# Optimization experiments

Measured on AMD Instinct MI355X. Metric: run time of the kernel, lower is better.

## Reference

```python
import jax, jax.numpy as jnp
import numpy as np

B, T, D, H = 4, 2048, 2048, 16
HD = D // H

def setup_inputs() -> dict:
    key = jax.random.key(0)
    k1, k2, k3 = jax.random.split(key, 3)
    x = jax.random.normal(k1, (B, T, D), dtype=jnp.float32)
    mask = jnp.ones((B, T), dtype=jnp.int32)
    # torch Linear weights, scaled like default init (~1/sqrt(fan_in))
    w_qkv = jax.random.normal(k2, (3 * D, D), dtype=jnp.float32) / np.sqrt(D)
    w_o = jax.random.normal(k3, (D, D), dtype=jnp.float32) / np.sqrt(D)
    return {"x": x, "mask": mask, "w_qkv": w_qkv, "w_o": w_o}

def reference(x, mask, w_qkv, w_o):
    # qkv projection: (B,T,D) @ (D,3D) -> (B,T,3D)
    qkv = jnp.einsum('btd,ed->bte', x, w_qkv)
    q, k, v = jnp.split(qkv, 3, axis=-1)
    # (B,T,D) -> (B,H,T,HD)
    def to_heads(t):
        return t.reshape(B, T, H, HD).transpose(0, 2, 1, 3)
    q, k, v = to_heads(q), to_heads(k), to_heads(v)
    scale = 1.0 / np.sqrt(HD).astype(np.float32)
    att = jnp.einsum('bhqd,bhkd->bhqk', q, k) * scale  # (B,H,T,T)
    att = jnp.where(mask[:, None, None, :] == 0, -jnp.inf, att)
    att = jax.nn.softmax(att, axis=-1)
    y = jnp.einsum('bhqk,bhkd->bhqd', att, v)  # (B,H,T,HD)
    y = y.transpose(0, 2, 1, 3).reshape(B, T, D)
    return jnp.einsum('btd,ed->bte', y, w_o)
```

## Files before the change

### kernel.cpp

```cpp
#include <hip/hip_runtime.h>
#include <hip/hip_bf16.h>

typedef __bf16 bf16;
typedef bf16 bf16x8 __attribute__((ext_vector_type(8)));
typedef float f32x4 __attribute__((ext_vector_type(4)));

struct alignas(8) bh4 { bf16 v[4]; };

__device__ __forceinline__ void glds16(const bf16* g, bf16* l) {
  __builtin_amdgcn_global_load_lds(
      (const __attribute__((address_space(1))) void*)g,
      (__attribute__((address_space(3))) void*)l, 16, 0, 0);
}

#define QSCALE (1.4426950408889634f / 11.313708498984761f)
#define DEFER_THR 8.0f

__global__ void convert_to_bf16(const float* __restrict__ s, bf16* __restrict__ dst,
                                long n) {
  const long stride = (long)gridDim.x * blockDim.x * 8;
  for (long i = ((long)blockIdx.x * blockDim.x + threadIdx.x) * 8; i < n; i += stride) {
    float4 a = *(const float4*)(s + i);
    float4 b = *(const float4*)(s + i + 4);
    bf16x8 o;
    o[0] = (bf16)a.x; o[1] = (bf16)a.y; o[2] = (bf16)a.z; o[3] = (bf16)a.w;
    o[4] = (bf16)b.x; o[5] = (bf16)b.y; o[6] = (bf16)b.z; o[7] = (bf16)b.w;
    *(bf16x8*)(dst + i) = o;
  }
}

template <int MODE>
__global__ void gemm_bt(const bf16* __restrict__ A, const bf16* __restrict__ Bw,
                        void* __restrict__ C0v, bf16* __restrict__ C1,
                        bf16* __restrict__ C2, int M, int N, int K) {
  __shared__ __align__(16) bf16 sA[128 * 32];
  __shared__ __align__(16) bf16 sB[128 * 32];
  const int tid = threadIdx.x;
  const int lane = tid & 63, wid = tid >> 6;
  const int wm = wid & 1, wn = wid >> 1;
  const int quad = lane >> 4, l16 = lane & 15;
  const int bm = blockIdx.y * 128, bn = blockIdx.x * 128;

  f32x4 acc[4][4] = {};

  const int srow = tid >> 2, scol = (tid & 3) << 3;
  const bf16* gA = A + (size_t)(bm + srow) * K + scol;
  const bf16* gB = Bw + (size_t)(bn + srow) * K + scol;
  const size_t row64 = (size_t)64 * K;

  for (int k0 = 0; k0 < K; k0 += 32) {
    glds16(gA + k0, &sA[tid * 8]);
    glds16(gA + k0 + row64, &sA[2048 + tid * 8]);
    glds16(gB + k0, &sB[tid * 8]);
    glds16(gB + k0 + row64, &sB[2048 + tid * 8]);
    __syncthreads();
    bf16x8 af[4], bff[4];
#pragma unroll
    for (int mt = 0; mt < 4; ++mt)
      af[mt] = *(const bf16x8*)&sA[(wm * 64 + mt * 16 + l16) * 32 + quad * 8];
#pragma unroll
    for (int nt = 0; nt < 4; ++nt)
      bff[nt] = *(const bf16x8*)&sB[(wn * 64 + nt * 16 + l16) * 32 + quad * 8];
#pragma unroll
    for (int mt = 0; mt < 4; ++mt)
#pragma unroll
      for (int nt = 0; nt < 4; ++nt)
        acc[mt][nt] = __builtin_amdgcn_mfma_f32_16x16x32_bf16(af[mt], bff[nt], acc[mt][nt], 0, 0, 0);
    __syncthreads();
  }

  if (MODE == 0) {
    bf16* C0 = (bf16*)C0v;
    const int which = blockIdx.x >> 4;
    const int h = blockIdx.x & 15;
#pragma unroll
    for (int mt = 0; mt < 4; ++mt) {
      const int m0 = bm + wm * 64 + mt * 16 + quad * 4;
      const int b = m0 >> 11, t0 = m0 & 2047;
#pragma unroll
      for (int nt = 0; nt < 4; ++nt) {
        const int hd = wn * 64 + nt * 16 + l16;
        if (which == 0) {
          bf16* dst = C0 + (((size_t)(b * 16 + h) * 2048 + t0) * 128 + hd);
#pragma unroll
          for (int r = 0; r < 4; ++r) dst[(size_t)r * 128] = (bf16)(acc[mt][nt][r] * QSCALE);
        } else if (which == 1) {
          bf16* dst = C1 + (((size_t)(b * 16 + h) * 2048 + t0) * 128 + hd);
#pragma unroll
          for (int r = 0; r < 4; ++r) dst[(size_t)r * 128] = (bf16)acc[mt][nt][r];
        } else {
          bh4 pk;
#pragma unroll
          for (int r = 0; r < 4; ++r) pk.v[r] = (bf16)acc[mt][nt][r];
          *(bh4*)(C2 + ((size_t)((b * 16 + h) * 128 + hd) * 2048 + t0)) = pk;
        }
      }
    }
  } else {
    float* C0 = (float*)C0v;
#pragma unroll
    for (int mt = 0; mt < 4; ++mt) {
      const int m0 = bm + wm * 64 + mt * 16 + quad * 4;
#pragma unroll
      for (int nt = 0; nt < 4; ++nt) {
        const int n = bn + wn * 64 + nt * 16 + l16;
#pragma unroll
        for (int r = 0; r < 4; ++r)
          C0[(size_t)(m0 + r) * N + n] = acc[mt][nt][r];
      }
    }
  }
}

__global__ __launch_bounds__(256, 3)
void attn_kernel(const bf16* __restrict__ Q, const bf16* __restrict__ Kb,
                 const bf16* __restrict__ Vt, const int* __restrict__ mask,
                 bf16* __restrict__ Y) {
  __shared__ __align__(16) bf16 smem[25600];
  bf16* sK = smem;
  bf16* sV = smem + 8192;
  bf16* sP = smem + 16384;

  const int tid = threadIdx.x;
  const int lane = tid & 63, w = tid >> 6;
  const int quad = lane >> 4, l16 = lane & 15;
  const int bh = blockIdx.x, b = bh >> 4, h = bh & 15;
  const int qt = blockIdx.y;
  const size_t head = (size_t)bh * (2048 * 128);

  bf16x8 qf[2][4];
#pragma unroll
  for (int nt = 0; nt < 2; ++nt) {
    const int t = qt * 128 + w * 32 + nt * 16 + l16;
    const bf16* g = Q + head + (size_t)t * 128 + quad * 8;
#pragma unroll
    for (int kk = 0; kk < 4; ++kk)
      qf[nt][kk] = *(const bf16x8*)(g + kk * 32);
  }

  f32x4 o[8][2] = {};
  float mrow[2] = {-3.0e38f, -3.0e38f};
  float lrow[2] = {0.0f, 0.0f};

  const int* maskb = mask + b * 2048;
  bf16* sPw = sP + w * (32 * 72);

  unsigned long long vmask;
  {
    const int4* mp4 = (const int4*)maskb;
    bool ok = true;
#pragma unroll
    for (int j = 0; j < 8; ++j) {
      const int4 q4 = mp4[lane * 8 + j];
      ok = ok && (q4.x != 0) && (q4.y != 0) && (q4.z != 0) && (q4.w != 0);
    }
    vmask = __ballot(ok);
  }

  for (int kt = 0; kt < 32; ++kt) {
    const int key0 = kt * 64;
    {
      const int cp = lane & 15;
      const int rbase = w * 16 + (lane >> 4);
#pragma unroll
      for (int p = 0; p < 4; ++p) {
        const int row = rbase + p * 4;
        const int c = (cp & 8) | ((cp ^ row) & 7);
        glds16(Kb + head + (size_t)(key0 + row) * 128 + c * 8,
               &sK[(w * 16 + p * 4) * 128 + lane * 8]);
      }
    }
    {
      const int cp = lane & 7;
      const int rbase = w * 32 + (lane >> 3);
#pragma unroll
      for (int p = 0; p < 4; ++p) {
        const int row = rbase + p * 8;
        const int c = cp ^ (row & 7);
        glds16(Vt + head + (size_t)row * 2048 + key0 + c * 8,
               &sV[(w * 32 + p * 8) * 64 + lane * 8]);
      }
    }
    __syncthreads();

    f32x4 st[4][2] = {};
#pragma unroll
    for (int kk = 0; kk < 4; ++kk) {
      bf16x8 ak[4];
#pragma unroll
      for (int mt = 0; mt < 4; ++mt) {
        const int row = mt * 16 + l16;
        const int c = kk * 4 + quad;
        const int cp = (c & 8) | ((c ^ row) & 7);
        ak[mt] = *(const bf16x8*)&sK[row * 128 + cp * 8];
      }
#pragma unroll
      for (int mt = 0; mt < 4; ++mt)
#pragma unroll
        for (int nt = 0; nt < 2; ++nt)
          st[mt][nt] = __builtin_amdgcn_mfma_f32_16x16x32_bf16(ak[mt], qf[nt][kk], st[mt][nt], 0, 0, 0);
    }

    if (((vmask >> (2 * kt)) & 3ULL) != 3ULL) {
#pragma unroll
      for (int mt = 0; mt < 4; ++mt) {
#pragma unroll
        for (int r = 0; r < 4; ++r) {
          const int mk = maskb[key0 + mt * 16 + quad * 4 + r];
#pragma unroll
          for (int nt = 0; nt < 2; ++nt)
            if (mk == 0) { st[mt][nt][r] = -1.0e30f; }
        }
      }
    }

#pragma unroll
    for (int nt = 0; nt < 2; ++nt) {
      float mx = -1.0e30f;
#pragma unroll
      for (int mt = 0; mt < 4; ++mt)
#pragma unroll
        for (int r = 0; r < 4; ++r) mx = fmaxf(mx, st[mt][nt][r]);
      mx = fmaxf(mx, __shfl_xor(mx, 16));
      mx = fmaxf(mx, __shfl_xor(mx, 32));
      if (!__all(mx <= mrow[nt] + DEFER_THR)) {
        const float newm = fmaxf(mrow[nt], mx);
        const float alpha = exp2f(mrow[nt] - newm);
        mrow[nt] = newm;
        lrow[nt] *= alpha;
#pragma unroll
        for (int mt = 0; mt < 8; ++mt)
#pragma unroll
          for (int r = 0; r < 4; ++r) o[mt][nt][r] *= alpha;
      }
      const float m = mrow[nt];
      float rs = 0.0f;
#pragma unroll
      for (int mt = 0; mt < 4; ++mt) {
        bh4 pk;
#pragma unroll
        for (int r = 0; r < 4; ++r) {
          const float p = exp2f(st[mt][nt][r] - m);
          rs += p;
          pk.v[r] = (bf16)p;
        }
        *(bh4*)&sPw[(nt * 16 + l16) * 72 + mt * 16 + quad * 4] = pk;
      }
      rs += __shfl_xor(rs, 16);
      rs += __shfl_xor(rs, 32);
      lrow[nt] += rs;
    }

#pragma unroll
    for (int kk = 0; kk < 2; ++kk) {
      bf16x8 bp[2];
#pragma unroll
      for (int nt = 0; nt < 2; ++nt)
        bp[nt] = *(const bf16x8*)&sPw[(nt * 16 + l16) * 72 + kk * 32 + quad * 8];
#pragma unroll
      for (int mt = 0; mt < 8; ++mt) {
        const int row = mt * 16 + l16;
        const int c = kk * 4 + quad;
        bf16x8 av = *(const bf16x8*)&sV[row * 64 + (c ^ (row & 7)) * 8];
#pragma unroll
        for (int nt = 0; nt < 2; ++nt)
          o[mt][nt] = __builtin_amdgcn_mfma_f32_16x16x32_bf16(av, bp[nt], o[mt][nt], 0, 0, 0);
      }
    }
    __syncthreads();
  }

  bf16* sOw = smem + w * 4352;
#pragma unroll
  for (int nt = 0; nt < 2; ++nt) {
    const float inv = 1.0f / lrow[nt];
#pragma unroll
    for (int mt = 0; mt < 8; ++mt) {
      bh4 pk;
#pragma unroll
      for (int r = 0; r < 4; ++r) pk.v[r] = (bf16)(o[mt][nt][r] * inv);
      *(bh4*)&sOw[(nt * 16 + l16) * 136 + mt * 16 + quad * 4] = pk;
    }
  }
  {
    const int col = (lane & 15) * 8;
#pragma unroll
    for (int p = 0; p < 8; ++p) {
      const int row = p * 4 + (lane >> 4);
      int4 v = *(const int4*)&sOw[row * 136 + col];
      const int token = qt * 128 + w * 32 + row;
      *(int4*)(Y + ((size_t)(b * 2048 + token)) * 2048 + h * 128 + col) = v;
    }
  }
}

extern "C" void kernel_launch(void* const* d_in, const int* in_sizes, int n_in,
                              void* d_out, int out_size, void* d_ws, size_t ws_size,
                              hipStream_t stream) {
  const float* x_raw  = (const float*)d_in[0];
  const int*   mask   = (const int*)d_in[1];
  const float* wq_raw = (const float*)d_in[2];
  const float* wo_raw = (const float*)d_in[3];
  float* out = (float*)d_out;

  char* ws = (char*)d_ws;
  const size_t MB = 1024 * 1024;
  bf16* xb  = (bf16*)(ws + 256);
  bf16* wqb = (bf16*)(ws + 256 + 32 * MB);
  bf16* qb  = (bf16*)(ws + 256 + 56 * MB);
  bf16* kb  = (bf16*)(ws + 256 + 88 * MB);
  bf16* vt  = (bf16*)(ws + 256 + 120 * MB);
  bf16* yb  = xb;
  bf16* wob = wqb;

  convert_to_bf16<<<1024, 256, 0, stream>>>(x_raw, xb, (long)in_sizes[0]);
  convert_to_bf16<<<1024, 256, 0, stream>>>(wq_raw, wqb, (long)in_sizes[2]);

  gemm_bt<0><<<dim3(48, 64), 256, 0, stream>>>(xb, wqb, qb, kb, vt, 8192, 6144, 2048);

  convert_to_bf16<<<1024, 256, 0, stream>>>(wo_raw, wob, (long)in_sizes[3]);

  attn_kernel<<<dim3(64, 16), 256, 0, stream>>>(qb, kb, vt, mask, yb);

  gemm_bt<1><<<dim3(16, 64), 256, 0, stream>>>(yb, wob, out, nullptr, nullptr, 8192, 2048, 2048);
}
```

Baseline: 670.7 us.

## Replace 128x128 GEMM with double-buffered 256x256 tile kernel using swizzled LDS

After: 632.5 us. 5.7% less time.

```diff
diff --git a/kernel.cpp b/kernel.cpp
--- a/kernel.cpp
+++ b/kernel.cpp
@@ -30,68 +30,165 @@
 }
 
 template <int MODE>
-__global__ void gemm_bt(const bf16* __restrict__ A, const bf16* __restrict__ Bw,
-                        void* __restrict__ C0v, bf16* __restrict__ C1,
-                        bf16* __restrict__ C2, int M, int N, int K) {
-  __shared__ __align__(16) bf16 sA[128 * 32];
-  __shared__ __align__(16) bf16 sB[128 * 32];
+__global__ __launch_bounds__(512, 2)
+void gemm256(const bf16* __restrict__ A, const bf16* __restrict__ Bw,
+             void* __restrict__ C0v, bf16* __restrict__ C1,
+             bf16* __restrict__ C2, int M, int N, int K) {
+  __shared__ __align__(16) bf16 sA[2][256 * 64];
+  __shared__ __align__(16) bf16 sB[2][256 * 64];
   const int tid = threadIdx.x;
-  const int lane = tid & 63, wid = tid >> 6;
-  const int wm = wid & 1, wn = wid >> 1;
+  const int lane = tid & 63;
+  const int wid = tid >> 6;
+  const int wm = wid >> 2, wn = wid & 3;
   const int quad = lane >> 4, l16 = lane & 15;
-  const int bm = blockIdx.y * 128, bn = blockIdx.x * 128;
-
-  f32x4 acc[4][4] = {};
-
-  const int srow = tid >> 2, scol = (tid & 3) << 3;
-  const bf16* gA = A + (size_t)(bm + srow) * K + scol;
-  const bf16* gB = Bw + (size_t)(bn + srow) * K + scol;
-  const size_t row64 = (size_t)64 * K;
-
-  for (int k0 = 0; k0 < K; k0 += 32) {
-    glds16(gA + k0, &sA[tid * 8]);
-    glds16(gA + k0 + row64, &sA[2048 + tid * 8]);
-    glds16(gB + k0, &sB[tid * 8]);
-    glds16(gB + k0 + row64, &sB[2048 + tid * 8]);
-    __syncthreads();
-    bf16x8 af[4], bff[4];
+
+  const int gx = gridDim.x;
+  const int nwg = gx * gridDim.y;
+  const int bid0 = blockIdx.y * gx + blockIdx.x;
+  const int cpx = nwg >> 3;
+  const int bid = (bid0 & 7) * cpx + (bid0 >> 3);
+  const int bm = (bid / gx) * 256, bn = (bid % gx) * 256;
+
+  f32x4 acc[8][4] = {};
+
+#pragma unroll
+  for (int r = 0; r < 4; ++r) {
+    const int idx = r * 512 + tid;
+    const int row = idx >> 3, cp = idx & 7;
+    const int cs = cp ^ (row & 7);
+    glds16(A + (size_t)(bm + row) * K + cs * 8, &sA[0][idx * 8]);
+    glds16(Bw + (size_t)(bn + row) * K + cs * 8, &sB[0][idx * 8]);
+  }
+  asm volatile("s_waitcnt vmcnt(0)" ::: "memory");
+  __builtin_amdgcn_s_barrier();
+
+  const int NT = K >> 6;
+  for (int kt = 0; kt < NT; ++kt) {
+    const bf16* cA = sA[kt & 1];
+    const bf16* cB = sB[kt & 1];
+    bf16x8 af[4][2];
+    bf16x8 bfA[2][2], bfB[2][2];
+
+#pragma unroll
+    for (int mt = 0; mt < 4; ++mt) {
+      const int R = wm * 128 + mt * 16 + l16;
+#pragma unroll
+      for (int s = 0; s < 2; ++s)
+        af[mt][s] = *(const bf16x8*)&cA[R * 64 + (((s * 4 + quad) ^ (R & 7)) * 8)];
+    }
+#pragma unroll
+    for (int nt = 0; nt < 2; ++nt) {
+      const int R = wn * 64 + nt * 16 + l16;
+#pragma unroll
+      for (int s = 0; s < 2; ++s)
+        bfA[nt][s] = *(const bf16x8*)&cB[R * 64 + (((s * 4 + quad) ^ (R & 7)) * 8)];
+    }
+    if (kt + 1 < NT) {
+      bf16* nA = (bf16*)sA[(kt + 1) & 1];
+      bf16* nB = (bf16*)sB[(kt + 1) & 1];
+      const int k0 = (kt + 1) << 6;
+#pragma unroll
+      for (int r = 0; r < 4; ++r) {
+        const int idx = r * 512 + tid;
+        const int row = idx >> 3, cp = idx & 7;
+        const int cs = cp ^ (row & 7);
+        glds16(A + (size_t)(bm + row) * K + k0 + cs * 8, &nA[idx * 8]);
+        glds16(Bw + (size_t)(bn + row) * K + k0 + cs * 8, &nB[idx * 8]);
+      }
+    }
+    __builtin_amdgcn_s_barrier();
+    asm volatile("s_waitcnt lgkmcnt(0)" ::: "memory");
+    __builtin_amdgcn_sched_barrier(0);
+    __builtin_amdgcn_s_setprio(1);
 #pragma unroll
     for (int mt = 0; mt < 4; ++mt)
-      af[mt] = *(const bf16x8*)&sA[(wm * 64 + mt * 16 + l16) * 32 + quad * 8];
-#pragma unroll
-    for (int nt = 0; nt < 4; ++nt)
-      bff[nt] = *(const bf16x8*)&sB[(wn * 64 + nt * 16 + l16) * 32 + quad * 8];
+#pragma unroll
+      for (int nt = 0; nt < 2; ++nt)
+#pragma unroll
+        for (int s = 0; s < 2; ++s)
+          acc[mt][nt] = __builtin_amdgcn_mfma_f32_16x16x32_bf16(af[mt][s], bfA[nt][s], acc[mt][nt], 0, 0, 0);
+    __builtin_amdgcn_s_setprio(0);
+    __builtin_amdgcn_s_barrier();
+
+#pragma unroll
+    for (int nt = 0; nt < 2; ++nt) {
+      const int R = wn * 64 + (2 + nt) * 16 + l16;
+#pragma unroll
+      for (int s = 0; s < 2; ++s)
+        bfB[nt][s] = *(const bf16x8*)&cB[R * 64 + (((s * 4 + quad) ^ (R & 7)) * 8)];
+    }
+    __builtin_amdgcn_s_barrier();
+    asm volatile("s_waitcnt lgkmcnt(0)" ::: "memory");
+    __builtin_amdgcn_sched_barrier(0);
+    __builtin_amdgcn_s_setprio(1);
 #pragma unroll
     for (int mt = 0; mt < 4; ++mt)
 #pragma unroll
-      for (int nt = 0; nt < 4; ++nt)
-        acc[mt][nt] = __builtin_amdgcn_mfma_f32_16x16x32_bf16(af[mt], bff[nt], acc[mt][nt], 0, 0, 0);
-    __syncthreads();
+      for (int nt = 0; nt < 2; ++nt)
+#pragma unroll
+        for (int s = 0; s < 2; ++s)
+          acc[mt][2 + nt] = __builtin_amdgcn_mfma_f32_16x16x32_bf16(af[mt][s], bfB[nt][s], acc[mt][2 + nt], 0, 0, 0);
+    __builtin_amdgcn_s_setprio(0);
+    __builtin_amdgcn_s_barrier();
+
+#pragma unroll
+    for (int mt = 0; mt < 4; ++mt) {
+      const int R = wm * 128 + 64 + mt * 16 + l16;
+#pragma unroll
+      for (int s = 0; s < 2; ++s)
+        af[mt][s] = *(const bf16x8*)&cA[R * 64 + (((s * 4 + quad) ^ (R & 7)) * 8)];
+    }
+    __builtin_amdgcn_s_barrier();
+    asm volatile("s_waitcnt lgkmcnt(0)" ::: "memory");
+    __builtin_amdgcn_sched_barrier(0);
+    __builtin_amdgcn_s_setprio(1);
+#pragma unroll
+    for (int mt = 0; mt < 4; ++mt)
+#pragma unroll
+      for (int nt = 0; nt < 2; ++nt)
+#pragma unroll
+        for (int s = 0; s < 2; ++s)
+          acc[4 + mt][nt] = __builtin_amdgcn_mfma_f32_16x16x32_bf16(af[mt][s], bfA[nt][s], acc[4 + mt][nt], 0, 0, 0);
+    __builtin_amdgcn_s_setprio(0);
+    __builtin_amdgcn_s_barrier();
+
+    __builtin_amdgcn_s_setprio(1);
+#pragma unroll
+    for (int mt = 0; mt < 4; ++mt)
+#pragma unroll
+      for (int nt = 0; nt < 2; ++nt)
+#pragma unroll
+        for (int s = 0; s < 2; ++s)
+          acc[4 + mt][2 + nt] = __builtin_amdgcn_mfma_f32_16x16x32_bf16(af[mt][s], bfB[nt][s], acc[4 + mt][2 + nt], 0, 0, 0);
+    __builtin_amdgcn_s_setprio(0);
+    asm volatile("s_waitcnt vmcnt(0)" ::: "memory");
+    __builtin_amdgcn_s_barrier();
   }
 
   if (MODE == 0) {
     bf16* C0 = (bf16*)C0v;
-    const int which = blockIdx.x >> 4;
-    const int h = blockIdx.x & 15;
-#pragma unroll
-    for (int mt = 0; mt < 4; ++mt) {
-      const int m0 = bm + wm * 64 + mt * 16 + quad * 4;
+#pragma unroll
+    for (int i = 0; i < 8; ++i) {
+      const int m0 = bm + wm * 128 + i * 16 + quad * 4;
       const int b = m0 >> 11, t0 = m0 & 2047;
 #pragma unroll
-      for (int nt = 0; nt < 4; ++nt) {
-        const int hd = wn * 64 + nt * 16 + l16;
+      for (int j = 0; j < 4; ++j) {
+        const int ncol = bn + wn * 64 + j * 16 + l16;
+        const int which = ncol >> 11;
+        const int d = ncol & 2047;
+        const int h = d >> 7, hd = d & 127;
         if (which == 0) {
           bf16* dst = C0 + (((size_t)(b * 16 + h) * 2048 + t0) * 128 + hd);
 #pragma unroll
-          for (int r = 0; r < 4; ++r) dst[(size_t)r * 128] = (bf16)(acc[mt][nt][r] * QSCALE);
+          for (int r = 0; r < 4; ++r) dst[(size_t)r * 128] = (bf16)(acc[i][j][r] * QSCALE);
         } else if (which == 1) {
           bf16* dst = C1 + (((size_t)(b * 16 + h) * 2048 + t0) * 128 + hd);
 #pragma unroll
-          for (int r = 0; r < 4; ++r) dst[(size_t)r * 128] = (bf16)acc[mt][nt][r];
+          for (int r = 0; r < 4; ++r) dst[(size_t)r * 128] = (bf16)acc[i][j][r];
         } else {
           bh4 pk;
 #pragma unroll
-          for (int r = 0; r < 4; ++r) pk.v[r] = (bf16)acc[mt][nt][r];
+          for (int r = 0; r < 4; ++r) pk.v[r] = (bf16)acc[i][j][r];
           *(bh4*)(C2 + ((size_t)((b * 16 + h) * 128 + hd) * 2048 + t0)) = pk;
         }
       }
@@ -99,14 +196,14 @@
   } else {
     float* C0 = (float*)C0v;
 #pragma unroll
-    for (int mt = 0; mt < 4; ++mt) {
-      const int m0 = bm + wm * 64 + mt * 16 + quad * 4;
-#pragma unroll
-      for (int nt = 0; nt < 4; ++nt) {
-        const int n = bn + wn * 64 + nt * 16 + l16;
+    for (int i = 0; i < 8; ++i) {
+      const int m0 = bm + wm * 128 + i * 16 + quad * 4;
+#pragma unroll
+      for (int j = 0; j < 4; ++j) {
+        const int n = bn + wn * 64 + j * 16 + l16;
 #pragma unroll
         for (int r = 0; r < 4; ++r)
-          C0[(size_t)(m0 + r) * N + n] = acc[mt][nt][r];
+          C0[(size_t)(m0 + r) * N + n] = acc[i][j][r];
       }
     }
   }
@@ -316,11 +413,11 @@
   convert_to_bf16<<<1024, 256, 0, stream>>>(x_raw, xb, (long)in_sizes[0]);
   convert_to_bf16<<<1024, 256, 0, stream>>>(wq_raw, wqb, (long)in_sizes[2]);
 
-  gemm_bt<0><<<dim3(48, 64), 256, 0, stream>>>(xb, wqb, qb, kb, vt, 8192, 6144, 2048);
+  gemm256<0><<<dim3(24, 32), 512, 0, stream>>>(xb, wqb, qb, kb, vt, 8192, 6144, 2048);
 
   convert_to_bf16<<<1024, 256, 0, stream>>>(wo_raw, wob, (long)in_sizes[3]);
 
   attn_kernel<<<dim3(64, 16), 256, 0, stream>>>(qb, kb, vt, mask, yb);
 
-  gemm_bt<1><<<dim3(16, 64), 256, 0, stream>>>(yb, wob, out, nullptr, nullptr, 8192, 2048, 2048);
+  gemm256<1><<<dim3(8, 32), 512, 0, stream>>>(yb, wob, out, nullptr, nullptr, 8192, 2048, 2048);
 }
```
